# Kernel tuning notes

Measured on AMD Instinct MI355X. Metric: run time of the kernel, lower is better.

Reference implementation:

```python
import jax, jax.numpy as jnp
import numpy as np

LC, LQ, BATCH, D = 1024, 512, 64, 256

def setup_inputs() -> dict:
    key = jax.random.key(0)
    k1, k2, k3, k4, k5 = jax.random.split(key, 5)
    return {
        "C": jax.random.normal(k1, (LC, BATCH, D), dtype=jnp.float32),
        "Q": jax.random.normal(k2, (LQ, BATCH, D), dtype=jnp.float32),
        "w4C": jax.random.normal(k3, (D, 1), dtype=jnp.float32) * 0.05,
        "w4Q": jax.random.normal(k4, (D, 1), dtype=jnp.float32) * 0.05,
        "w4mlu": jax.random.normal(k5, (1, 1, D), dtype=jnp.float32) * 0.05,
        "bias": jnp.zeros((1,), dtype=jnp.float32),
    }

def reference(C, Q, w4C, w4Q, w4mlu, bias):
    # seq-major -> batch-major: (L, B, D) -> (B, L, D)
    C = jnp.transpose(C, (1, 0, 2))  # (B, Lc, D)
    Q = jnp.transpose(Q, (1, 0, 2))  # (B, Lq, D)
    # trilinear attention scores (dropout is identity in eval mode)
    sub0 = C @ w4C                                      # (B, Lc, 1)
    sub1 = jnp.transpose(Q @ w4Q, (0, 2, 1))            # (B, 1, Lq)
    sub2 = jnp.einsum('bcd,bqd->bcq', C * w4mlu, Q)     # (B, Lc, Lq)
    S = sub0 + sub1 + sub2 + bias                       # (B, Lc, Lq)
    S1 = jax.nn.softmax(S, axis=2)   # row softmax over query positions
    S2 = jax.nn.softmax(S, axis=1)   # col softmax over context positions
    A = jnp.einsum('bcq,bqd->bcd', S1, Q)               # (B, Lc, D)
    B_ = jnp.einsum('bck,bqk->bcq', S1, S2)             # S1 @ S2^T : (B, Lc, Lc)
    B_ = jnp.einsum('bce,bed->bcd', B_, C)              # (B, Lc, D)
    out = jnp.concatenate([C, A, C * A, C * B_], axis=2)  # (B, Lc, 4D)
    return jnp.transpose(out, (0, 2, 1))                  # (B, 4D, Lc)
```

## Files before the change

### kernel.cpp

```cpp
#include <hip/hip_runtime.h>

#define LCc 1024
#define LQq 512
#define BB  64
#define DDim 256

typedef __attribute__((ext_vector_type(8))) short bf16x8;
typedef __attribute__((ext_vector_type(4))) float f32x4;
typedef __attribute__((ext_vector_type(4))) unsigned short us4;
typedef __attribute__((ext_vector_type(8))) unsigned short us8;

static __device__ __forceinline__ unsigned short f2b(float f) {
  unsigned u = __builtin_bit_cast(unsigned, f);
  unsigned r = u + 0x7FFFu + ((u >> 16) & 1u);
  return (unsigned short)(r >> 16);
}
static __device__ __forceinline__ bf16x8 ldb8(const unsigned short* p) {
  return *(const bf16x8*)p;
}
static __device__ __forceinline__ f32x4 MFMA16(bf16x8 a, bf16x8 b, f32x4 c) {
  return __builtin_amdgcn_mfma_f32_16x16x32_bf16(a, b, c, 0, 0, 0);
}
static __device__ __forceinline__ void gload16(const unsigned short* g, unsigned short* l) {
  __builtin_amdgcn_global_load_lds(
      (const __attribute__((address_space(1))) unsigned int*)g,
      (__attribute__((address_space(3))) unsigned int*)l, 16, 0, 0);
}

__global__ __launch_bounds__(256, 4) void prep_CF(const float* __restrict__ C,
    const float* __restrict__ w4C, const float* __restrict__ w4mlu,
    unsigned short* __restrict__ Cw, unsigned short* __restrict__ CT,
    float* __restrict__ rowAdd) {
  __shared__ unsigned short tile[64][65];
  int c0 = blockIdx.x * 64, b = blockIdx.y;
  int t = threadIdx.x, r = t >> 2, g = t & 3;
  float rsum = 0.f;
  for (int dch = 0; dch < 4; dch++) {
    int d0 = dch * 64;
    const float* src = C + ((size_t)(c0 + r) * BB + b) * DDim + d0 + g * 16;
    unsigned short cwv[16];
    #pragma unroll
    for (int i = 0; i < 4; i++) {
      float4 v = ((const float4*)src)[i];
      float4 wm = *(const float4*)(w4mlu + d0 + g * 16 + i * 4);
      float4 wc = *(const float4*)(w4C + d0 + g * 16 + i * 4);
      rsum += v.x * wc.x + v.y * wc.y + v.z * wc.z + v.w * wc.w;
      cwv[i * 4 + 0] = f2b(v.x * wm.x);
      cwv[i * 4 + 1] = f2b(v.y * wm.y);
      cwv[i * 4 + 2] = f2b(v.z * wm.z);
      cwv[i * 4 + 3] = f2b(v.w * wm.w);
      tile[r][g * 16 + i * 4 + 0] = f2b(v.x);
      tile[r][g * 16 + i * 4 + 1] = f2b(v.y);
      tile[r][g * 16 + i * 4 + 2] = f2b(v.z);
      tile[r][g * 16 + i * 4 + 3] = f2b(v.w);
    }
    unsigned short* cwp = Cw + ((size_t)((b << 10) + c0 + r)) * DDim + d0 + g * 16;
    *(us8*)cwp = *(us8*)&cwv[0];
    *(us8*)(cwp + 8) = *(us8*)&cwv[8];
    __syncthreads();
    unsigned short* ctp = CT + ((size_t)((b << 8) + d0 + r)) * LCc + c0 + g * 16;
    us8 o0, o1;
    #pragma unroll
    for (int j = 0; j < 8; j++) { o0[j] = tile[g * 16 + j][r]; o1[j] = tile[g * 16 + 8 + j][r]; }
    *(us8*)ctp = o0;
    *(us8*)(ctp + 8) = o1;
    __syncthreads();
  }
  rsum += __shfl_xor(rsum, 1);
  rsum += __shfl_xor(rsum, 2);
  if (g == 0) rowAdd[((size_t)b << 10) + c0 + r] = rsum;
}

__global__ __launch_bounds__(256, 4) void prep_QF(const float* __restrict__ Q,
    const float* __restrict__ w4Q, const float* __restrict__ bias,
    unsigned short* __restrict__ Qb, unsigned short* __restrict__ QT,
    float* __restrict__ colAdd, float* __restrict__ colL) {
  __shared__ unsigned short tile[64][65];
  int q0 = blockIdx.x * 64, b = blockIdx.y;
  int t = threadIdx.x, r = t >> 2, g = t & 3;
  float rsum = 0.f;
  for (int dch = 0; dch < 4; dch++) {
    int d0 = dch * 64;
    const float* src = Q + ((size_t)(q0 + r) * BB + b) * DDim + d0 + g * 16;
    #pragma unroll
    for (int i = 0; i < 4; i++) {
      float4 v = ((const float4*)src)[i];
      float4 wq = *(const float4*)(w4Q + d0 + g * 16 + i * 4);
      rsum += v.x * wq.x + v.y * wq.y + v.z * wq.z + v.w * wq.w;
      tile[r][g * 16 + i * 4 + 0] = f2b(v.x);
      tile[r][g * 16 + i * 4 + 1] = f2b(v.y);
      tile[r][g * 16 + i * 4 + 2] = f2b(v.z);
      tile[r][g * 16 + i * 4 + 3] = f2b(v.w);
    }
    __syncthreads();
    unsigned short* qbp = Qb + ((size_t)((b << 9) + q0 + r)) * DDim + d0 + g * 16;
    us8 s0, s1;
    #pragma unroll
    for (int j = 0; j < 8; j++) { s0[j] = tile[r][g * 16 + j]; s1[j] = tile[r][g * 16 + 8 + j]; }
    *(us8*)qbp = s0;
    *(us8*)(qbp + 8) = s1;
    unsigned short* qtp = QT + ((size_t)((b << 8) + d0 + r)) * LQq + q0 + g * 16;
    us8 o0, o1;
    #pragma unroll
    for (int j = 0; j < 8; j++) { o0[j] = tile[g * 16 + j][r]; o1[j] = tile[g * 16 + 8 + j][r]; }
    *(us8*)qtp = o0;
    *(us8*)(qtp + 8) = o1;
    __syncthreads();
  }
  rsum += __shfl_xor(rsum, 1);
  rsum += __shfl_xor(rsum, 2);
  if (g == 0) {
    colAdd[((size_t)b << 9) + q0 + r] = rsum + bias[0];
    colL[((size_t)b << 9) + q0 + r] = 0.0f;
  }
}

__global__ __launch_bounds__(256, 3) void k_P(const unsigned short* __restrict__ Cw,
    const unsigned short* __restrict__ Qb, const float* __restrict__ rowAdd,
    const float* __restrict__ colAdd, unsigned short* __restrict__ Pt,
    float* __restrict__ rowL, float* __restrict__ colL) {
  int blk = blockIdx.x;
  int b = blk >> 4, ct = blk & 15;
  int t = threadIdx.x, w = t >> 6, lane = t & 63;
  int col = lane & 15, quad = lane >> 4;
  int c0w = ct * 64 + w * 16;
  __shared__ unsigned short tile[2][64][40];
  __shared__ float colAcc[LQq];
  for (int i = t; i < LQq; i += 256) colAcc[i] = 0.f;
  __syncthreads();

  bf16x8 afrag[8];
  const unsigned short* aPtr = Cw + ((size_t)((b << 10) + c0w + col)) * DDim + quad * 8;
  #pragma unroll
  for (int kk = 0; kk < 8; kk++) afrag[kk] = ldb8(aPtr + kk * 32);
  float rAddv[4];
  #pragma unroll
  for (int r = 0; r < 4; r++) rAddv[r] = rowAdd[((size_t)b << 10) + c0w + quad * 4 + r];
  float rowSum[4] = {0.f, 0.f, 0.f, 0.f};

  int cur = 0;
  for (int win = 0; win < 16; win++) {
    #pragma unroll
    for (int h = 0; h < 2; h++) {
      int q0 = win * 32 + h * 16;
      const unsigned short* bPtr = Qb + ((size_t)((b << 9) + q0 + col)) * DDim + quad * 8;
      f32x4 acc = {0.f, 0.f, 0.f, 0.f};
      #pragma unroll
      for (int kk = 0; kk < 8; kk++) acc = MFMA16(afrag[kk], ldb8(bPtr + kk * 32), acc);
      float cAdd = colAdd[((size_t)b << 9) + q0 + col];
      float csum = 0.f;
      #pragma unroll
      for (int r = 0; r < 4; r++) {
        float e = __expf(acc[r] + rAddv[r] + cAdd);
        rowSum[r] += e;
        csum += e;
        tile[cur][w * 16 + quad * 4 + r][h * 16 + col] = f2b(e);
      }
      csum += __shfl_xor(csum, 16);
      csum += __shfl_xor(csum, 32);
      if (lane < 16) atomicAdd(&colAcc[q0 + lane], csum);
    }
    __syncthreads();
    us8 frag = *(const us8*)&tile[cur][w * 16 + col][quad * 8];
    *(us8*)(Pt + (((size_t)(b * 64 + ct * 4 + w) * 16 + win) << 9) + lane * 8) = frag;
    cur ^= 1;
  }
  #pragma unroll
  for (int r = 0; r < 4; r++) {
    float s = rowSum[r];
    s += __shfl_xor(s, 1); s += __shfl_xor(s, 2);
    s += __shfl_xor(s, 4); s += __shfl_xor(s, 8);
    if (col == 0) rowL[((size_t)b << 10) + c0w + quad * 4 + r] = s;
  }
  __syncthreads();
  for (int i = t; i < LQq; i += 256) atomicAdd(&colL[((size_t)b << 9) + i], colAcc[i]);
}

__global__ __launch_bounds__(256, 4) void k_T(const unsigned short* __restrict__ Pt,
    const unsigned short* __restrict__ CT, const float* __restrict__ colL,
    unsigned short* __restrict__ TT) {
  int blk = blockIdx.x;
  int b = blk >> 4, qs = blk & 15;
  int t = threadIdx.x, w = t >> 6, lane = t & 63;
  int col = lane & 15, quad = lane >> 4;
  int dq = w * 64;
  int cbl = w & 1, jh = w >> 1;
  __shared__ unsigned short pT[32][40];

  f32x4 accT[2][4];
  #pragma unroll
  for (int mf = 0; mf < 2; mf++)
    #pragma unroll
    for (int nf = 0; nf < 4; nf++) accT[mf][nf] = (f32x4){0.f, 0.f, 0.f, 0.f};

  us8 frag = *(const us8*)(Pt + (((size_t)(b * 64 + 0 * 2 + cbl) * 16 + qs) << 9) + lane * 8);
  for (int cs = 0; cs < 32; cs++) {
    bf16x8 bf[4];
    #pragma unroll
    for (int nf = 0; nf < 4; nf++)
      bf[nf] = ldb8(CT + ((size_t)((b << 8) + dq + nf * 16 + col)) * LCc + cs * 32 + quad * 8);
    #pragma unroll
    for (int jj = 0; jj < 4; jj++) {
      int j = jh * 4 + jj;
      pT[quad * 8 + j][cbl * 16 + col] = (unsigned short)frag[j];
    }
    __syncthreads();
    bf16x8 pa[2];
    #pragma unroll
    for (int mf = 0; mf < 2; mf++) pa[mf] = *(const bf16x8*)&pT[mf * 16 + col][quad * 8];
    #pragma unroll
    for (int mf = 0; mf < 2; mf++)
      #pragma unroll
      for (int nf = 0; nf < 4; nf++) accT[mf][nf] = MFMA16(pa[mf], bf[nf], accT[mf][nf]);
    if (cs < 31)
      frag = *(const us8*)(Pt + (((size_t)(b * 64 + (cs + 1) * 2 + cbl) * 16 + qs) << 9) + lane * 8);
    __syncthreads();
  }
  float cInv[2][4];
  #pragma unroll
  for (int mf = 0; mf < 2; mf++)
    #pragma unroll
    for (int r = 0; r < 4; r++)
      cInv[mf][r] = 1.0f / colL[((size_t)b << 9) + qs * 32 + mf * 16 + quad * 4 + r];
  #pragma unroll
  for (int mf = 0; mf < 2; mf++)
    #pragma unroll
    for (int nf = 0; nf < 4; nf++) {
      us4 ov;
      #pragma unroll
      for (int r = 0; r < 4; r++) ov[r] = f2b(accT[mf][nf][r] * cInv[mf][r]);
      *(us4*)(TT + ((size_t)((b << 8) + dq + nf * 16 + col)) * LQq + qs * 32 + mf * 16 + quad * 4) = ov;
    }
}

__global__ __launch_bounds__(256, 2) void k_AB(const unsigned short* __restrict__ Pt,
    const unsigned short* __restrict__ QT, const unsigned short* __restrict__ TT,
    const float* __restrict__ rowL, const float* __restrict__ C,
    float* __restrict__ out) {
  int blk = blockIdx.x;
  int b = blk >> 4, ct = blk & 15;
  int t = threadIdx.x, w = t >> 6, lane = t & 63;
  int col = lane & 15, quad = lane >> 4;
  int dq = w * 64;
  __shared__ unsigned short sb[4][2][8][512];

  f32x4 accA[4][4], accB[4][4];
  #pragma unroll
  for (int mf = 0; mf < 4; mf++)
    #pragma unroll
    for (int nf = 0; nf < 4; nf++) {
      accA[mf][nf] = (f32x4){0.f, 0.f, 0.f, 0.f};
      accB[mf][nf] = (f32x4){0.f, 0.f, 0.f, 0.f};
    }

  #define STAGE(qs_, buf_)                                                              \
    {                                                                                   \
      int _q = (qs_) * 32 + quad * 8;                                                   \
      _Pragma("unroll")                                                                 \
      for (int nf = 0; nf < 4; nf++) {                                                  \
        size_t rowD = (size_t)((b << 8) + dq + nf * 16 + col);                          \
        gload16(QT + (rowD << 9) + _q, &sb[w][buf_][nf][0]);                            \
        gload16(TT + (rowD << 9) + _q, &sb[w][buf_][4 + nf][0]);                        \
      }                                                                                 \
    }
  #define PTLOAD(qs_, set_)                                                             \
    {                                                                                   \
      _Pragma("unroll")                                                                 \
      for (int mf = 0; mf < 4; mf++)                                                    \
        pa[set_][mf] = ldb8(ptB + mf * 8192 + (qs_) * 512);                             \
    }
  #define SBAR __builtin_amdgcn_sched_barrier(0)

  const unsigned short* ptB = Pt + (((size_t)(b * 64 + ct * 4) * 16) << 9) + lane * 8;
  bf16x8 pa[3][4];

  SBAR;
  STAGE(0, 0);
  SBAR;
  PTLOAD(0, 0);
  SBAR;
  PTLOAD(1, 1);
  SBAR;

  #pragma unroll
  for (int qs = 0; qs < 16; qs++) {
    if (qs < 15) { STAGE(qs + 1, (qs + 1) & 1); }
    SBAR;
    if (qs < 14) { PTLOAD(qs + 2, (qs + 2) % 3); }
    SBAR;
    if (qs < 14)      asm volatile("s_waitcnt vmcnt(16)" ::: "memory");
    else if (qs == 14) asm volatile("s_waitcnt vmcnt(12)" ::: "memory");
    else               asm volatile("s_waitcnt vmcnt(0)" ::: "memory");
    SBAR;
    bf16x8 bq[4], bt[4];
    #pragma unroll
    for (int nf = 0; nf < 4; nf++) {
      bq[nf] = ldb8(&sb[w][qs & 1][nf][lane * 8]);
      bt[nf] = ldb8(&sb[w][qs & 1][4 + nf][lane * 8]);
    }
    #pragma unroll
    for (int mf = 0; mf < 4; mf++)
      #pragma unroll
      for (int nf = 0; nf < 4; nf++) {
        accA[mf][nf] = MFMA16(pa[qs % 3][mf], bq[nf], accA[mf][nf]);
        accB[mf][nf] = MFMA16(pa[qs % 3][mf], bt[nf], accB[mf][nf]);
      }
  }

  float rInv[4][4];
  #pragma unroll
  for (int mf = 0; mf < 4; mf++) {
    float4 rv = *(const float4*)(rowL + ((size_t)b << 10) + ct * 64 + mf * 16 + quad * 4);
    rInv[mf][0] = 1.0f / rv.x; rInv[mf][1] = 1.0f / rv.y;
    rInv[mf][2] = 1.0f / rv.z; rInv[mf][3] = 1.0f / rv.w;
  }
  size_t outB = (size_t)b << 20;
  #pragma unroll
  for (int mf = 0; mf < 4; mf++) {
    int cc = ct * 64 + mf * 16 + quad * 4;
    #pragma unroll
    for (int nf = 0; nf < 4; nf++) {
      int d = dq + nf * 16 + col;
      float4 vC, vA, vCA, vCB;
      #pragma unroll
      for (int r = 0; r < 4; r++) {
        float Cv = C[((size_t)(cc + r) * BB + b) * DDim + d];
        float Av = accA[mf][nf][r] * rInv[mf][r];
        float Bv = accB[mf][nf][r] * rInv[mf][r];
        ((float*)&vC)[r] = Cv;
        ((float*)&vA)[r] = Av;
        ((float*)&vCA)[r] = Cv * Av;
        ((float*)&vCB)[r] = Cv * Bv;
      }
      float* o0 = out + outB + (size_t)d * LCc + cc;
      *(float4*)(o0) = vC;
      *(float4*)(o0 + (size_t)DDim * LCc) = vA;
      *(float4*)(o0 + 2 * (size_t)DDim * LCc) = vCA;
      *(float4*)(o0 + 3 * (size_t)DDim * LCc) = vCB;
    }
  }
  #undef STAGE
  #undef PTLOAD
  #undef SBAR
}

extern "C" void kernel_launch(void* const* d_in, const int* in_sizes, int n_in,
                              void* d_out, int out_size, void* d_ws, size_t ws_size,
                              hipStream_t stream) {
  const float* C    = (const float*)d_in[0];
  const float* Q    = (const float*)d_in[1];
  const float* w4C  = (const float*)d_in[2];
  const float* w4Q  = (const float*)d_in[3];
  const float* w4mlu= (const float*)d_in[4];
  const float* bias = (const float*)d_in[5];
  float* out = (float*)d_out;
  char* ws = (char*)d_ws;

  unsigned short* Cw = (unsigned short*)(ws);
  unsigned short* CT = (unsigned short*)(ws + 33554432);
  unsigned short* Qb = (unsigned short*)(ws + 67108864);
  unsigned short* TT = Qb;
  unsigned short* QT = (unsigned short*)(ws + 83886080);
  unsigned short* Pt = (unsigned short*)(ws + 100663296);
  float* rowAdd = (float*)(ws + 167772160);
  float* colAdd = (float*)(ws + 168034304);
  float* rowL   = (float*)(ws + 168165376);
  float* colL   = (float*)(ws + 168427520);

  prep_CF<<<dim3(LCc / 64, BB), 256, 0, stream>>>(C, w4C, w4mlu, Cw, CT, rowAdd);
  prep_QF<<<dim3(LQq / 64, BB), 256, 0, stream>>>(Q, w4Q, bias, Qb, QT, colAdd, colL);
  k_P<<<BB * 16, 256, 0, stream>>>(Cw, Qb, rowAdd, colAdd, Pt, rowL, colL);
  k_T<<<BB * 16, 256, 0, stream>>>(Pt, CT, colL, TT);
  k_AB<<<BB * 16, 256, 0, stream>>>(Pt, QT, TT, rowL, C, out);
}
```

Measured before the change: 699.8 us.

## Remap blocks to XCDs by batch and halve k_AB tile for occupancy

Block indices in k_P, k_T and k_AB are remapped so that blocks sharing a batch land on the same XCD (round-robin dispatch modulo 8). This is meant to improve L2 reuse of per-batch data such as Pt, QT and TT. k_AB now covers 32 context rows per block instead of 64, with a single LDS buffer, two P fragments instead of three, occupancy raised to 4, and twice as many blocks. The pipeline is reordered to wait, read LDS, issue the next stage, then run MFMAs. The smaller tile means more global reads of QT and TT per output, and single buffering adds waits in exchange for higher occupancy.

```diff
diff --git a/kernel.cpp b/kernel.cpp
--- a/kernel.cpp
+++ b/kernel.cpp
@@ -119,8 +119,9 @@
     const unsigned short* __restrict__ Qb, const float* __restrict__ rowAdd,
     const float* __restrict__ colAdd, unsigned short* __restrict__ Pt,
     float* __restrict__ rowL, float* __restrict__ colL) {
-  int blk = blockIdx.x;
-  int b = blk >> 4, ct = blk & 15;
+  int idx = blockIdx.x;
+  int xcd = idx & 7, loc = idx >> 3;
+  int b = xcd * 8 + (loc >> 4), ct = loc & 15;
   int t = threadIdx.x, w = t >> 6, lane = t & 63;
   int col = lane & 15, quad = lane >> 4;
   int c0w = ct * 64 + w * 16;
@@ -179,8 +180,9 @@
 __global__ __launch_bounds__(256, 4) void k_T(const unsigned short* __restrict__ Pt,
     const unsigned short* __restrict__ CT, const float* __restrict__ colL,
     unsigned short* __restrict__ TT) {
-  int blk = blockIdx.x;
-  int b = blk >> 4, qs = blk & 15;
+  int idx = blockIdx.x;
+  int xcd = idx & 7, loc = idx >> 3;
+  int b = xcd * 8 + (loc >> 4), qs = loc & 15;
   int t = threadIdx.x, w = t >> 6, lane = t & 63;
   int col = lane & 15, quad = lane >> 4;
   int dq = w * 64;
@@ -233,49 +235,50 @@
     }
 }
 
-__global__ __launch_bounds__(256, 2) void k_AB(const unsigned short* __restrict__ Pt,
+__global__ __launch_bounds__(256, 4) void k_AB(const unsigned short* __restrict__ Pt,
     const unsigned short* __restrict__ QT, const unsigned short* __restrict__ TT,
     const float* __restrict__ rowL, const float* __restrict__ C,
     float* __restrict__ out) {
-  int blk = blockIdx.x;
-  int b = blk >> 4, ct = blk & 15;
+  int idx = blockIdx.x;
+  int xcd = idx & 7, loc = idx >> 3;
+  int b = xcd * 8 + (loc >> 5), ct = loc & 31;
   int t = threadIdx.x, w = t >> 6, lane = t & 63;
   int col = lane & 15, quad = lane >> 4;
   int dq = w * 64;
-  __shared__ unsigned short sb[4][2][8][512];
-
-  f32x4 accA[4][4], accB[4][4];
-  #pragma unroll
-  for (int mf = 0; mf < 4; mf++)
+  __shared__ unsigned short sb[4][8][512];
+
+  f32x4 accA[2][4], accB[2][4];
+  #pragma unroll
+  for (int mf = 0; mf < 2; mf++)
     #pragma unroll
     for (int nf = 0; nf < 4; nf++) {
       accA[mf][nf] = (f32x4){0.f, 0.f, 0.f, 0.f};
       accB[mf][nf] = (f32x4){0.f, 0.f, 0.f, 0.f};
     }
 
-  #define STAGE(qs_, buf_)                                                              \
+  #define STAGE(qs_)                                                                    \
     {                                                                                   \
       int _q = (qs_) * 32 + quad * 8;                                                   \
       _Pragma("unroll")                                                                 \
       for (int nf = 0; nf < 4; nf++) {                                                  \
         size_t rowD = (size_t)((b << 8) + dq + nf * 16 + col);                          \
-        gload16(QT + (rowD << 9) + _q, &sb[w][buf_][nf][0]);                            \
-        gload16(TT + (rowD << 9) + _q, &sb[w][buf_][4 + nf][0]);                        \
+        gload16(QT + (rowD << 9) + _q, &sb[w][nf][0]);                                  \
+        gload16(TT + (rowD << 9) + _q, &sb[w][4 + nf][0]);                              \
       }                                                                                 \
     }
   #define PTLOAD(qs_, set_)                                                             \
     {                                                                                   \
       _Pragma("unroll")                                                                 \
-      for (int mf = 0; mf < 4; mf++)                                                    \
+      for (int mf = 0; mf < 2; mf++)                                                    \
         pa[set_][mf] = ldb8(ptB + mf * 8192 + (qs_) * 512);                             \
     }
   #define SBAR __builtin_amdgcn_sched_barrier(0)
 
-  const unsigned short* ptB = Pt + (((size_t)(b * 64 + ct * 4) * 16) << 9) + lane * 8;
-  bf16x8 pa[3][4];
+  const unsigned short* ptB = Pt + (((size_t)(b * 64 + ct * 2) * 16) << 9) + lane * 8;
+  bf16x8 pa[2][2];
 
   SBAR;
-  STAGE(0, 0);
+  STAGE(0);
   SBAR;
   PTLOAD(0, 0);
   SBAR;
@@ -284,40 +287,42 @@
 
   #pragma unroll
   for (int qs = 0; qs < 16; qs++) {
-    if (qs < 15) { STAGE(qs + 1, (qs + 1) & 1); }
-    SBAR;
-    if (qs < 14) { PTLOAD(qs + 2, (qs + 2) % 3); }
-    SBAR;
-    if (qs < 14)      asm volatile("s_waitcnt vmcnt(16)" ::: "memory");
-    else if (qs == 14) asm volatile("s_waitcnt vmcnt(12)" ::: "memory");
-    else               asm volatile("s_waitcnt vmcnt(0)" ::: "memory");
+    if (qs < 15) asm volatile("s_waitcnt vmcnt(2)" ::: "memory");
+    else         asm volatile("s_waitcnt vmcnt(0)" ::: "memory");
     SBAR;
     bf16x8 bq[4], bt[4];
     #pragma unroll
     for (int nf = 0; nf < 4; nf++) {
-      bq[nf] = ldb8(&sb[w][qs & 1][nf][lane * 8]);
-      bt[nf] = ldb8(&sb[w][qs & 1][4 + nf][lane * 8]);
-    }
-    #pragma unroll
-    for (int mf = 0; mf < 4; mf++)
+      bq[nf] = ldb8(&sb[w][nf][lane * 8]);
+      bt[nf] = ldb8(&sb[w][4 + nf][lane * 8]);
+    }
+    asm volatile("s_waitcnt lgkmcnt(0)" ::: "memory");
+    SBAR;
+    if (qs < 15) { STAGE(qs + 1); }
+    SBAR;
+    #pragma unroll
+    for (int mf = 0; mf < 2; mf++)
       #pragma unroll
       for (int nf = 0; nf < 4; nf++) {
-        accA[mf][nf] = MFMA16(pa[qs % 3][mf], bq[nf], accA[mf][nf]);
-        accB[mf][nf] = MFMA16(pa[qs % 3][mf], bt[nf], accB[mf][nf]);
+        accA[mf][nf] = MFMA16(pa[qs & 1][mf], bq[nf], accA[mf][nf]);
+        accB[mf][nf] = MFMA16(pa[qs & 1][mf], bt[nf], accB[mf][nf]);
       }
-  }
-
-  float rInv[4][4];
-  #pragma unroll
-  for (int mf = 0; mf < 4; mf++) {
-    float4 rv = *(const float4*)(rowL + ((size_t)b << 10) + ct * 64 + mf * 16 + quad * 4);
+    SBAR;
+    if (qs < 14) { PTLOAD(qs + 2, qs & 1); }
+    SBAR;
+  }
+
+  float rInv[2][4];
+  #pragma unroll
+  for (int mf = 0; mf < 2; mf++) {
+    float4 rv = *(const float4*)(rowL + ((size_t)b << 10) + ct * 32 + mf * 16 + quad * 4);
     rInv[mf][0] = 1.0f / rv.x; rInv[mf][1] = 1.0f / rv.y;
     rInv[mf][2] = 1.0f / rv.z; rInv[mf][3] = 1.0f / rv.w;
   }
   size_t outB = (size_t)b << 20;
   #pragma unroll
-  for (int mf = 0; mf < 4; mf++) {
-    int cc = ct * 64 + mf * 16 + quad * 4;
+  for (int mf = 0; mf < 2; mf++) {
+    int cc = ct * 32 + mf * 16 + quad * 4;
     #pragma unroll
     for (int nf = 0; nf < 4; nf++) {
       int d = dq + nf * 16 + col;
@@ -371,5 +376,5 @@
   prep_QF<<<dim3(LQq / 64, BB), 256, 0, stream>>>(Q, w4Q, bias, Qb, QT, colAdd, colL);
   k_P<<<BB * 16, 256, 0, stream>>>(Cw, Qb, rowAdd, colAdd, Pt, rowL, colL);
   k_T<<<BB * 16, 256, 0, stream>>>(Pt, CT, colL, TT);
-  k_AB<<<BB * 16, 256, 0, stream>>>(Pt, QT, TT, rowL, C, out);
-}
+  k_AB<<<BB * 32, 256, 0, stream>>>(Pt, QT, TT, rowL, C, out);
+}
```

Result: slower. 905.2 us (+29.3%).
